# Performance work log

Measured on AMD Instinct MI355X. Metric: run time of the kernel, lower is better.

## Reference

```python
import jax, jax.numpy as jnp
import numpy as np

EPS = 1e-8  # torch.nn.CosineSimilarity default eps
VOCAB, D = 100000, 300
S, A, W = 256, 256, 8


def setup_inputs() -> dict:
    key = jax.random.key(0)
    k1, k2, k3 = jax.random.split(key, 3)
    emb = jax.random.normal(k1, (VOCAB, D), dtype=jnp.float32)
    sen_cats = jax.random.randint(k2, (S, W), 0, VOCAB, dtype=jnp.int64)
    ann_cats = jax.random.randint(k3, (A, W), 0, VOCAB, dtype=jnp.int64)
    return {"emb": emb, "sen_cats": sen_cats, "ann_cats": ann_cats, "none_idx": 0}


def _forward(emb, sen_cats, ann_cats, none_idx):
    sen_e = emb[sen_cats]            # [S, W, D] per-word embeddings (get_cat_emb)
    ann_e = emb[ann_cats]            # [A, W, D]
    none_emb = emb[none_idx]         # [D]

    # cosine similarity for every (sen word, ann word) pair: [S, A, W, W]
    dots = jnp.einsum('swd,avd->sawv', sen_e, ann_e)
    ns = jnp.linalg.norm(sen_e, axis=-1)   # [S, W]
    na = jnp.linalg.norm(ann_e, axis=-1)   # [A, W]
    denom = jnp.maximum(ns[:, None, :, None] * na[None, :, None, :], EPS)
    cos = dots / denom

    # sen word equal to none embedding -> sim forced to 0 (torch.equal branch)
    sen_none = jnp.all(sen_e == none_emb, axis=-1)             # [S, W]
    sim = jnp.where(sen_none[:, None, :, None], jnp.zeros((), cos.dtype), cos)

    # faithful order-dependent running update: start 0;
    # max_sim = sim if (sim >= max_sim or sim < 0); sen word is outer loop.
    n_pairs = sim.shape[2] * sim.shape[3]
    sims_seq = sim.reshape(sim.shape[0], sim.shape[1], n_pairs).transpose(2, 0, 1)  # [W*W, S, A]

    def step(cur, s):
        new = jnp.where((s >= cur) | (s < 0), s, cur)
        return new, None

    max_sim, _ = jax.lax.scan(step, jnp.zeros(sim.shape[:2], sim.dtype), sims_seq)  # [S, A]

    sen_wd_emb = sen_e.sum(axis=1)  # [S, D] (stack(...).sum(0) per sen category)
    return max_sim, sen_wd_emb


def reference(emb, sen_cats, ann_cats, none_idx):
    return _forward(emb, sen_cats, ann_cats, none_idx)
```

## Files before the change

### kernel.cpp

```cpp
#include <hip/hip_runtime.h>
#include <hip/hip_fp16.h>

#define D 300
#define NS 256
#define NA 256
#define W 8
#define NROWS 2048
#define NCHUNK 10

typedef _Float16 half8 __attribute__((ext_vector_type(8)));
typedef float f32x4 __attribute__((ext_vector_type(4)));

__device__ __forceinline__ int swaddr(int rt, int lr, int k4) {
    int c = k4 >> 5, lk = (k4 & 31) >> 3, e = k4 & 7;
    return ((rt * NCHUNK + c) * 64 + lk * 16 + lr) * 8 + e;
}

__device__ __forceinline__ ushort4 cvt4(float4 v) {
    ushort4 h;
    h.x = __half_as_ushort(__float2half(v.x));
    h.y = __half_as_ushort(__float2half(v.y));
    h.z = __half_as_ushort(__float2half(v.z));
    h.w = __half_as_ushort(__float2half(v.w));
    return h;
}

__global__ __launch_bounds__(256) void k_gather(const float* __restrict__ emb,
                                                const int* __restrict__ sen_cats,
                                                const int* __restrict__ ann_cats,
                                                const int* __restrict__ none_idx,
                                                unsigned short* __restrict__ AH,
                                                unsigned short* __restrict__ BH,
                                                float* __restrict__ rsn,
                                                float* __restrict__ ran,
                                                int* __restrict__ sflag) {
    int tid = threadIdx.x;
    int wv = tid >> 6, lane = tid & 63;
    int task = blockIdx.x * 4 + wv;
    bool isSen = task < NROWS;
    int r = isSen ? task : task - NROWS;
    int cat = isSen ? sen_cats[r] : ann_cats[r];
    unsigned short* HI = isSen ? AH : BH;
    int rt = r >> 4, lr = r & 15;

    const float4* src = reinterpret_cast<const float4*>(emb + (size_t)cat * D);
    float4 v0 = src[lane];
    *reinterpret_cast<ushort4*>(HI + swaddr(rt, lr, lane * 4)) = cvt4(v0);
    double acc = (double)v0.x * v0.x + (double)v0.y * v0.y +
                 (double)v0.z * v0.z + (double)v0.w * v0.w;
    if (lane < 11) {
        float4 v1 = src[lane + 64];
        *reinterpret_cast<ushort4*>(HI + swaddr(rt, lr, (lane + 64) * 4)) = cvt4(v1);
        acc += (double)v1.x * v1.x + (double)v1.y * v1.y +
               (double)v1.z * v1.z + (double)v1.w * v1.w;
    } else if (lane < 16) {
        ushort4 z = {0, 0, 0, 0};
        *reinterpret_cast<ushort4*>(HI + swaddr(rt, lr, (lane + 64) * 4)) = z;
    }
    for (int off = 32; off > 0; off >>= 1) acc += __shfl_down(acc, off, 64);
    if (lane == 0) {
        float rn = (float)(1.0 / sqrt(acc));
        if (isSen) {
            rsn[r] = rn;
            sflag[r] = (cat == none_idx[0]) ? 1 : 0;
        } else {
            ran[r] = rn;
        }
    }
}

__global__ __launch_bounds__(128) void k_out2(const float* __restrict__ emb,
                                              const int* __restrict__ sen_cats,
                                              float* __restrict__ out2) {
    int b = blockIdx.x, i = threadIdx.x;
    if (i >= 75) return;
    float4 s = make_float4(0.f, 0.f, 0.f, 0.f);
#pragma unroll
    for (int w = 0; w < W; ++w) {
        int cat = sen_cats[b * W + w];
        float4 v = reinterpret_cast<const float4*>(emb + (size_t)cat * D)[i];
        s.x += v.x; s.y += v.y; s.z += v.z; s.w += v.w;
    }
    reinterpret_cast<float4*>(out2 + (size_t)b * D)[i] = s;
}

__global__ __launch_bounds__(256, 1) void k_main(const unsigned short* __restrict__ AHu,
                                                 const unsigned short* __restrict__ BHu,
                                                 const float* __restrict__ rsn,
                                                 const float* __restrict__ ran,
                                                 const int* __restrict__ sflag,
                                                 float* __restrict__ out) {
    const _Float16* AH = reinterpret_cast<const _Float16*>(AHu);
    const _Float16* BH = reinterpret_cast<const _Float16*>(BHu);

    __shared__ float cosld[128][128];

    int tid = threadIdx.x;
    int wv = tid >> 6, lane = tid & 63;
    int wy = wv >> 1, wx = wv & 1;
    int lr = lane & 15;
    int lk = lane >> 4;
    int by = blockIdx.y, bx = blockIdx.x;

    int aBase[4], bBase[4];
#pragma unroll
    for (int m = 0; m < 4; ++m)
        aBase[m] = (((by * 8 + wy * 4 + m) * NCHUNK) * 64 + lane) * 8;
#pragma unroll
    for (int n = 0; n < 4; ++n)
        bBase[n] = (((bx * 8 + wx * 4 + n) * NCHUNK) * 64 + lane) * 8;

    f32x4 acc[4][4] = {};
    half8 Ah[4], Bh[4];

#pragma unroll
    for (int c = 0; c < NCHUNK; ++c) {
        int co = c * 512;
#pragma unroll
        for (int m = 0; m < 4; ++m)
            Ah[m] = *reinterpret_cast<const half8*>(AH + aBase[m] + co);
#pragma unroll
        for (int n = 0; n < 4; ++n)
            Bh[n] = *reinterpret_cast<const half8*>(BH + bBase[n] + co);
#pragma unroll
        for (int m = 0; m < 4; ++m)
#pragma unroll
            for (int n = 0; n < 4; ++n)
                acc[m][n] = __builtin_amdgcn_mfma_f32_16x16x32_f16(Ah[m], Bh[n], acc[m][n], 0, 0, 0);
    }

#pragma unroll
    for (int m = 0; m < 4; ++m) {
        int rbase = wy * 64 + m * 16 + lk * 4;
#pragma unroll
        for (int r = 0; r < 4; ++r) {
            int grow = by * 128 + rbase + r;
            float rsv = rsn[grow];
            float fm = sflag[grow] ? 0.f : 1.f;
            float rf = rsv * fm;
#pragma unroll
            for (int n = 0; n < 4; ++n) {
                int lc = wx * 64 + n * 16 + lr;
                float rav = ran[bx * 128 + lc];
                cosld[rbase + r][lc] = acc[m][n][r] * rf * rav;
            }
        }
    }
    __syncthreads();

    int pi = tid >> 4, pj = tid & 15;
    float cur = 0.f;
#pragma unroll
    for (int w = 0; w < W; ++w) {
        const float* rowp = &cosld[pi * 8 + w][pj * 8];
#pragma unroll
        for (int v = 0; v < W; ++v) {
            float sv = rowp[v];
            cur = (sv >= cur || sv < 0.f) ? sv : cur;
        }
    }
    out[(by * 16 + pi) * NA + (bx * 16 + pj)] = cur;
}

extern "C" void kernel_launch(void* const* d_in, const int* in_sizes, int n_in,
                              void* d_out, int out_size, void* d_ws, size_t ws_size,
                              hipStream_t stream) {
    const float* emb = (const float*)d_in[0];
    const int* sen = (const int*)d_in[1];
    const int* ann = (const int*)d_in[2];
    const int* none = (const int*)d_in[3];
    float* out = (float*)d_out;

    char* ws = (char*)d_ws;
    unsigned short* AH = (unsigned short*)(ws + 0);
    unsigned short* BH = (unsigned short*)(ws + 1310720);
    float* rsn = (float*)(ws + 2621440);
    float* ran = (float*)(ws + 2629632);
    int* sflag = (int*)(ws + 2637824);

    hipLaunchKernelGGL(k_gather, dim3(1024), dim3(256), 0, stream,
                       emb, sen, ann, none, AH, BH, rsn, ran, sflag);
    hipLaunchKernelGGL(k_out2, dim3(NS), dim3(128), 0, stream,
                       emb, sen, out + NS * NA);
    hipLaunchKernelGGL(k_main, dim3(16, 16), dim3(256), 0, stream,
                       AH, BH, rsn, ran, sflag, out);
}
```

Before: 21.61 us.

## Stage MFMA operands through double-buffered LDS with register prefetch in k_main

New measurement: 41.78 us. +93.3%, slower.

```diff
diff --git a/kernel.cpp b/kernel.cpp
--- a/kernel.cpp
+++ b/kernel.cpp
@@ -93,7 +93,10 @@
     const _Float16* AH = reinterpret_cast<const _Float16*>(AHu);
     const _Float16* BH = reinterpret_cast<const _Float16*>(BHu);
 
-    __shared__ float cosld[128][128];
+    __shared__ union U {
+        struct { _Float16 A[2][8][64][8]; _Float16 B[2][8][64][8]; } s;
+        float cosld[128][128];
+    } u;
 
     int tid = threadIdx.x;
     int wv = tid >> 6, lane = tid & 63;
@@ -102,31 +105,65 @@
     int lk = lane >> 4;
     int by = blockIdx.y, bx = blockIdx.x;
 
-    int aBase[4], bBase[4];
-#pragma unroll
-    for (int m = 0; m < 4; ++m)
-        aBase[m] = (((by * 8 + wy * 4 + m) * NCHUNK) * 64 + lane) * 8;
-#pragma unroll
-    for (int n = 0; n < 4; ++n)
-        bBase[n] = (((bx * 8 + wx * 4 + n) * NCHUNK) * 64 + lane) * 8;
+    int q = tid >> 6, sl = tid & 63;
+    const _Float16* gsrc[4];
+#pragma unroll
+    for (int j = 0; j < 4; ++j) {
+        int i = q + j * 4;
+        gsrc[j] = (i < 8)
+            ? AH + (((by * 8 + i) * NCHUNK) * 64 + sl) * 8
+            : BH + (((bx * 8 + (i - 8)) * NCHUNK) * 64 + sl) * 8;
+    }
+
+    float4 rg0[4], rg1[4];
+
+#define LOADREG(rg, c)                                                       \
+    {                                                                        \
+        _Pragma("unroll")                                                    \
+        for (int j = 0; j < 4; ++j)                                          \
+            rg[j] = *reinterpret_cast<const float4*>(gsrc[j] + (c) * 512);   \
+    }
+#define DSWRITE(buf, rg)                                                     \
+    {                                                                        \
+        _Pragma("unroll")                                                    \
+        for (int j = 0; j < 4; ++j) {                                        \
+            int i = q + j * 4;                                               \
+            float4* dp = (i < 8)                                             \
+                ? reinterpret_cast<float4*>(&u.s.A[buf][i][sl][0])           \
+                : reinterpret_cast<float4*>(&u.s.B[buf][i - 8][sl][0]);      \
+            *dp = rg[j];                                                     \
+        }                                                                    \
+    }
 
     f32x4 acc[4][4] = {};
     half8 Ah[4], Bh[4];
 
+    LOADREG(rg0, 0);
+    LOADREG(rg1, 1);
+    DSWRITE(0, rg0);
+    __syncthreads();
+
 #pragma unroll
     for (int c = 0; c < NCHUNK; ++c) {
-        int co = c * 512;
+        int cur = c & 1;
+        if (c + 1 < NCHUNK) {
+            if (cur == 0) DSWRITE(1, rg1) else DSWRITE(0, rg0)
+        }
+        if (c + 2 < NCHUNK) {
+            if (cur == 0) LOADREG(rg0, c + 2) else LOADREG(rg1, c + 2)
+        }
 #pragma unroll
         for (int m = 0; m < 4; ++m)
-            Ah[m] = *reinterpret_cast<const half8*>(AH + aBase[m] + co);
+            Ah[m] = *reinterpret_cast<const half8*>(&u.s.A[cur][wy * 4 + m][lane][0]);
 #pragma unroll
         for (int n = 0; n < 4; ++n)
-            Bh[n] = *reinterpret_cast<const half8*>(BH + bBase[n] + co);
+            Bh[n] = *reinterpret_cast<const half8*>(&u.s.B[cur][wx * 4 + n][lane][0]);
 #pragma unroll
         for (int m = 0; m < 4; ++m)
 #pragma unroll
             for (int n = 0; n < 4; ++n)
                 acc[m][n] = __builtin_amdgcn_mfma_f32_16x16x32_f16(Ah[m], Bh[n], acc[m][n], 0, 0, 0);
+        __syncthreads();
     }
 
 #pragma unroll
@@ -142,7 +179,7 @@
             for (int n = 0; n < 4; ++n) {
                 int lc = wx * 64 + n * 16 + lr;
                 float rav = ran[bx * 128 + lc];
-                cosld[rbase + r][lc] = acc[m][n][r] * rf * rav;
+                u.cosld[rbase + r][lc] = acc[m][n][r] * rf * rav;
             }
         }
     }
@@ -152,7 +189,7 @@
     float cur = 0.f;
 #pragma unroll
     for (int w = 0; w < W; ++w) {
-        const float* rowp = &cosld[pi * 8 + w][pj * 8];
+        const float* rowp = &u.cosld[pi * 8 + w][pj * 8];
 #pragma unroll
         for (int v = 0; v < W; ++v) {
             float sv = rowp[v];
@@ -160,6 +197,8 @@
         }
     }
     out[(by * 16 + pi) * NA + (bx * 16 + pj)] = cur;
+#undef LOADREG
+#undef DSWRITE
 }
 
 extern "C" void kernel_launch(void* const* d_in, const int* in_sizes, int n_in,
```
